# Kernel tuning notes

Hardware: AMD Instinct MI355X
Metric: run time of the kernel (lower is better)

The kernel has to match this reference:

```python
import jax, jax.numpy as jnp
import numpy as np

D_SPEC, D_PRE, D_CTX, D_H = 552, 256, 128, 1024


def _lstm_cell(x, h, c, Wih, Whh, bih, bhh):
    # PyTorch gate order: i, f, g, o
    g = x @ Wih.T + bih + h @ Whh.T + bhh
    i, f, gg, o = jnp.split(g, 4, axis=-1)
    c_new = jax.nn.sigmoid(f) * c + jax.nn.sigmoid(i) * jnp.tanh(gg)
    h_new = jax.nn.sigmoid(o) * jnp.tanh(c_new)
    return h_new, c_new


def _conv1d(x, w, b):
    # x: [B, C_in, L], w: [C_out, C_in, K], 'same' padding for K=5
    y = jax.lax.conv_general_dilated(x, w, window_strides=(1,), padding=[(2, 2)],
                                     dimension_numbers=('NCH', 'OIH', 'NCH'))
    return y + b[None, :, None]


def setup_inputs() -> dict:
    key = jax.random.key(0)
    ks = jax.random.split(key, 26)
    s = 0.05
    shapes = {
        'S_pad': (600, 64, D_SPEC),
        'pre_W1': (D_PRE, D_SPEC), 'pre_b1': (D_PRE,),
        'pre_W2': (D_PRE, D_PRE), 'pre_b2': (D_PRE,),
        'Wih0': (4 * D_H, D_PRE + D_CTX), 'Whh0': (4 * D_H, D_H),
        'bih0': (4 * D_H,), 'bhh0': (4 * D_H,),
        'Wih1': (4 * D_H, D_H), 'Whh1': (4 * D_H, D_H),
        'bih1': (4 * D_H,), 'bhh1': (4 * D_H,),
        'lin_W': (D_SPEC, D_H + D_CTX), 'lin_b': (D_SPEC,),
        'cw1': (512, D_SPEC, 5), 'cb1': (512,),
        'cw2': (512, 512, 5), 'cb2': (512,),
        'cw3': (512, 512, 5), 'cb3': (512,),
        'cw4': (512, 512, 5), 'cb4': (512,),
        'cw5': (D_SPEC, 512, 5), 'cb5': (D_SPEC,),
    }
    out = {}
    for i, (name, shp) in enumerate(shapes.items()):
        scale = 1.0 if name == 'S_pad' else s
        out[name] = scale * jax.random.normal(ks[i], shp, dtype=jnp.float32)
    return out


def reference(S_pad, pre_W1, pre_b1, pre_W2, pre_b2,
              Wih0, Whh0, bih0, bhh0, Wih1, Whh1, bih1, bhh1,
              lin_W, lin_b, cw1, cb1, cw2, cb2, cw3, cb3, cw4, cb4, cw5, cb5):
    L, B, _ = S_pad.shape
    # teacher forcing: input frame at t is S_pad[t-1] (zeros at t=0) -> precompute pre_net batched
    in_frames = jnp.concatenate([jnp.zeros((1, B, D_SPEC), S_pad.dtype), S_pad[:-1]], axis=0)
    pre = jax.nn.relu(in_frames @ pre_W1.T + pre_b1)
    pre = jax.nn.relu(pre @ pre_W2.T + pre_b2)  # dropout = identity (eval)
    ctx = jnp.zeros((L, B, D_CTX), S_pad.dtype)  # dummy_context
    lstm_in = jnp.concatenate([pre, ctx], axis=-1)  # [L, B, 384]

    h0 = jnp.zeros((B, D_H), S_pad.dtype)
    init = (h0, h0, h0, h0)  # (h0, c0, h1, c1)

    def step(carry, x):
        h0, c0, h1, c1 = carry
        h0, c0 = _lstm_cell(x, h0, c0, Wih0, Whh0, bih0, bhh0)
        h1, c1 = _lstm_cell(h0, h1, c1, Wih1, Whh1, bih1, bhh1)
        return (h0, c0, h1, c1), h1

    _, outs = jax.lax.scan(step, init, lstm_in)  # [L, B, 1024]
    S_pred = jnp.concatenate([outs, ctx], axis=-1) @ lin_W.T + lin_b  # [L, B, 552]

    x = jnp.transpose(S_pred, (1, 2, 0))  # [B, 552, L]
    x = jnp.tanh(_conv1d(x, cw1, cb1))
    x = jnp.tanh(_conv1d(x, cw2, cb2))
    x = jnp.tanh(_conv1d(x, cw3, cb3))
    x = jnp.tanh(_conv1d(x, cw4, cb4))
    x = _conv1d(x, cw5, cb5)
    S_residual = jnp.transpose(x, (2, 0, 1))  # [L, B, 552]
    return S_pred + S_residual
```

## Files before the change

### kernel.cpp

```cpp
#include <hip/hip_runtime.h>
#include <cstdint>
#include <cstddef>

typedef __bf16 bf16;
typedef __attribute__((ext_vector_type(8))) __bf16 bf16x8;
typedef __attribute__((ext_vector_type(4))) float f32x4;
typedef __attribute__((ext_vector_type(4))) unsigned u32x4;

#define DEV static __device__ __forceinline__

DEV float sigm_(float x) { return 1.f / (1.f + __expf(-x)); }
DEV float tanhf_(float x) {
  float e = __expf(-2.f * fabsf(x));
  float t = (1.f - e) / (1.f + e);
  return x < 0.f ? -t : t;
}

DEV void gload_lds16(const bf16* g, bf16* l) {
  __builtin_amdgcn_global_load_lds((const __attribute__((address_space(1))) void*)g,
                                   (__attribute__((address_space(3))) void*)l, 16, 0, 0);
}

__global__ void k_frames(const float* __restrict__ S, bf16* __restrict__ dst) {
  int idx = blockIdx.x * 256 + threadIdx.x;
  if (idx >= 38400 * 576) return;
  int r = idx / 576, c = idx - r * 576;
  int t = r >> 6, b = r & 63;
  float v = (t == 0 || c >= 552) ? 0.f : S[((size_t)(t - 1) * 64 + b) * 552 + c];
  dst[idx] = (bf16)v;
}

__global__ void k_pad2d(const float* __restrict__ src, bf16* __restrict__ dst,
                        int N, int Cdst, int Csrc, int Rsrc, int sstride) {
  int idx = blockIdx.x * 256 + threadIdx.x;
  if (idx >= N) return;
  int r = idx / Cdst, c = idx - r * Cdst;
  float v = (r < Rsrc && c < Csrc) ? src[(size_t)r * sstride + c] : 0.f;
  dst[idx] = (bf16)v;
}

__global__ void k_w0c(const float* __restrict__ Whh0, const float* __restrict__ Wih0,
                      bf16* __restrict__ dst) {
  int idx = blockIdx.x * 256 + threadIdx.x;
  if (idx >= 4096 * 1280) return;
  int r = idx / 1280, k = idx - r * 1280;
  float v = (k < 1024) ? Whh0[(size_t)r * 1024 + k] : Wih0[(size_t)r * 384 + (k - 1024)];
  dst[idx] = (bf16)v;
}

__global__ void k_w1c(const float* __restrict__ Wih1, const float* __restrict__ Whh1,
                      bf16* __restrict__ dst) {
  int idx = blockIdx.x * 256 + threadIdx.x;
  if (idx >= 4096 * 2048) return;
  int r = idx / 2048, k = idx - r * 2048;
  float v = (k < 1024) ? Wih1[(size_t)r * 1024 + k] : Whh1[(size_t)r * 1024 + (k - 1024)];
  dst[idx] = (bf16)v;
}

__global__ void k_convw(const float* __restrict__ src, bf16* __restrict__ dst,
                        int N, int Cpad, int Cisrc, int Cosrc) {
  int idx = blockIdx.x * 256 + threadIdx.x;
  if (idx >= N) return;
  int per = 5 * Cpad;
  int co = idx / per, rem = idx - co * per;
  int tap = rem / Cpad, ci = rem - tap * Cpad;
  float v = (co < Cosrc && ci < Cisrc) ? src[((size_t)co * Cisrc + ci) * 5 + tap] : 0.f;
  dst[idx] = (bf16)v;
}

__global__ void k_zpad(bf16* __restrict__ X0, bf16* __restrict__ X1, bf16* __restrict__ X2) {
  int idx = blockIdx.x * 256 + threadIdx.x;
  if (idx >= 64 * 4 * 1600) return;
  int per = 4 * 1600;
  int b = idx / per, rem = idx - b * per;
  int rr = rem / 1600, c = rem - rr * 1600;
  int row = (rr < 2) ? rr : 600 + rr;
  if (c < 576) X0[((size_t)b * 604 + row) * 576 + c] = (bf16)0.f;
  else if (c < 1088) X1[((size_t)b * 604 + row) * 512 + (c - 576)] = (bf16)0.f;
  else X2[((size_t)b * 604 + row) * 512 + (c - 1088)] = (bf16)0.f;
}

__global__ void k_sent(unsigned* __restrict__ C0u) {
  int idx = blockIdx.x * 256 + threadIdx.x;
  if (idx >= 600 * 64 * 512) return;
  int d = idx & 511;
  int rb = idx >> 9;
  int b = rb & 63, t1 = (rb >> 6) + 1;
  C0u[(size_t)t1 * 40960 + (size_t)b * 640 + d] = 0xFFFFFFFFu;
}

enum { M_RELU = 0, M_LINEAR = 1, M_CONVT = 2, M_CONVF = 3 };

template <int MODE>
__global__ __launch_bounds__(256) void gemm_k(
    const bf16* __restrict__ A, const bf16* __restrict__ B, int Ktot, int Kstride,
    int Brows, const float* __restrict__ bias,
    bf16* __restrict__ outB, int outStride, int colP, int colOff,
    float* __restrict__ outF, bf16* __restrict__ outX) {
  const int tid = threadIdx.x;
  const int lane = tid & 63, wv = tid >> 6;
  const int n0 = blockIdx.x * 128, m0 = blockIdx.y * 128;
  const int bz = blockIdx.z;
  __shared__ bf16 As[128 * 64];
  __shared__ bf16 Bs[128 * 64];
  f32x4 acc[4][4] = {};
  const int wr = wv >> 1, wc = wv & 1;
  int tap = 0, ci0 = 0;

  for (int kb = 0; kb < Ktot; kb += 64) {
#pragma unroll
    for (int j = 0; j < 4; ++j) {
      int rt = wv * 32 + j * 8 + (lane >> 3);
      const bf16* gp;
      if (MODE == M_CONVT || MODE == M_CONVF) {
        int l = m0 + rt;
        if (l > 599) l = 599;
        gp = A + ((size_t)(bz * 604 + l + tap)) * Kstride + ci0 + (lane & 7) * 8;
      } else {
        gp = A + (size_t)(m0 + rt) * Kstride + kb + (lane & 7) * 8;
      }
      gload_lds16(gp, &As[(wv * 32 + j * 8) * 64]);
    }
#pragma unroll
    for (int j = 0; j < 4; ++j) {
      int rn = n0 + wv * 32 + j * 8 + (lane >> 3);
      if (rn >= Brows) rn = Brows - 1;
      const bf16* gp = B + (size_t)rn * Ktot + kb + (lane & 7) * 8;
      gload_lds16(gp, &Bs[(wv * 32 + j * 8) * 64]);
    }
    __syncthreads();
#pragma unroll
    for (int ks = 0; ks < 2; ++ks) {
      const int ko = ks * 32 + (lane >> 4) * 8;
      bf16x8 af[4], bfr[4];
#pragma unroll
      for (int i = 0; i < 4; ++i) {
        af[i] = *(const bf16x8*)&As[(wr * 64 + i * 16 + (lane & 15)) * 64 + ko];
        bfr[i] = *(const bf16x8*)&Bs[(wc * 64 + i * 16 + (lane & 15)) * 64 + ko];
      }
#pragma unroll
      for (int mi = 0; mi < 4; ++mi)
#pragma unroll
        for (int ni = 0; ni < 4; ++ni)
          acc[mi][ni] = __builtin_amdgcn_mfma_f32_16x16x32_bf16(af[mi], bfr[ni], acc[mi][ni], 0, 0, 0);
    }
    __syncthreads();
    ci0 += 64;
    if (ci0 == Kstride) { ci0 = 0; ++tap; }
  }

  const int r0 = (lane >> 4) * 4, cc = lane & 15;
#pragma unroll
  for (int mi = 0; mi < 4; ++mi) {
#pragma unroll
    for (int ni = 0; ni < 4; ++ni) {
#pragma unroll
      for (int r = 0; r < 4; ++r) {
        float v = acc[mi][ni][r];
        int gr = m0 + wr * 64 + mi * 16 + r0 + r;
        int gc = n0 + wc * 64 + ni * 16 + cc;
        if (MODE == M_RELU) {
          v += bias[gc];
          v = fmaxf(v, 0.f);
          outB[(size_t)(gr >> 6) * outStride + (size_t)(gr & 63) * colP + colOff + gc] = (bf16)v;
        } else if (MODE == M_LINEAR) {
          if (gc < 552) {
            v += bias[gc];
            int t = gr >> 6, b = gr & 63;
            outF[(size_t)gr * 552 + gc] = v;
            outX[((size_t)b * 604 + t + 2) * 576 + gc] = (bf16)v;
          }
        } else if (MODE == M_CONVT) {
          if (gr < 600) {
            v = tanhf_(v + bias[gc]);
            outB[((size_t)bz * 604 + gr + 2) * 512 + gc] = (bf16)v;
          }
        } else {
          if (gr < 600 && gc < 552) {
            v += bias[gc];
            float* p = outF + ((size_t)gr * 64 + bz) * 552 + gc;
            *p += v;
          }
        }
      }
    }
  }
}

template <int LAYER>
DEV void scan_impl(bf16* __restrict__ C0, bf16* __restrict__ H1,
                   const bf16* __restrict__ W, const float* __restrict__ bi,
                   const float* __restrict__ bh, float* gb, int u0, int b0) {
  constexpr int KT = LAYER ? 2048 : 1280;
  constexpr int NKS = KT / 256;
  const int tid = threadIdx.x, lane = tid & 63, w = tid >> 6;
  const int kb = w * (KT / 8);

  bf16x8 wreg[4][NKS];
#pragma unroll
  for (int gi = 0; gi < 4; ++gi)
#pragma unroll
    for (int ks = 0; ks < NKS; ++ks)
      wreg[gi][ks] = *(const bf16x8*)(W + (size_t)(gi * 1024 + u0 + (lane & 15)) * KT +
                                      kb + ks * 32 + (lane >> 4) * 8);

  const int uc = tid & 15, bl = tid >> 4;
  float bs[4];
#pragma unroll
  for (int g = 0; g < 4; ++g) bs[g] = bi[g * 1024 + u0 + uc] + bh[g * 1024 + u0 + uc];
  float cst = 0.f;
  const int rotc = (bl + 4 * uc) & 31;

  const int r0 = lane & 15, q8 = (lane >> 4) * 8;
  const int un = lane & 15, qb = (lane >> 4) * 4;

  for (int t = 0; t < 600; ++t) {
    const bf16* A0;
    int RS;
    if (!LAYER) {
      RS = 1280;
      A0 = C0 + (size_t)t * 81920 + (size_t)(b0 + r0) * 1280 + kb + q8;
    } else if (w < 4) {
      RS = 1280;
      A0 = C0 + (size_t)(t + 1) * 81920 + (size_t)(b0 + r0) * 1280 + kb + q8;
    } else {
      RS = 1024;
      A0 = H1 + (size_t)(t + 1) * 65536 + (size_t)(b0 + r0) * 1024 + (kb - 1024) + q8;
    }
    const bf16* A1 = A0 + 16 * RS;

    u32x4 va[NKS], vb[NKS];
    if (!LAYER) {
#pragma unroll
      for (int ks = 0; ks < NKS; ++ks)
        if (kb + ks * 32 >= 1024) {
          va[ks] = *(const u32x4*)(A0 + ks * 32);
          vb[ks] = *(const u32x4*)(A1 + ks * 32);
        }
    }
    for (;;) {
#pragma unroll
      for (int ks = 0; ks < NKS; ++ks) {
        if (LAYER || kb + ks * 32 < 1024) {
          asm volatile("global_load_dwordx4 %0, %1, off sc0 sc1"
                       : "=v"(va[ks]) : "v"(A0 + ks * 32) : "memory");
          asm volatile("global_load_dwordx4 %0, %1, off sc0 sc1"
                       : "=v"(vb[ks]) : "v"(A1 + ks * 32) : "memory");
        }
      }
      asm volatile("s_waitcnt vmcnt(0)" ::: "memory");
      __builtin_amdgcn_sched_barrier(0);
      unsigned bad = 0;
#pragma unroll
      for (int ks = 0; ks < NKS; ++ks) {
        if (LAYER || kb + ks * 32 < 1024) {
          bad |= (va[ks].x == 0xFFFFFFFFu) | (va[ks].y == 0xFFFFFFFFu) |
                 (va[ks].z == 0xFFFFFFFFu) | (va[ks].w == 0xFFFFFFFFu) |
                 (vb[ks].x == 0xFFFFFFFFu) | (vb[ks].y == 0xFFFFFFFFu) |
                 (vb[ks].z == 0xFFFFFFFFu) | (vb[ks].w == 0xFFFFFFFFu);
        }
      }
      if (!__ballot(bad)) break;
      __builtin_amdgcn_s_sleep(2);
    }

    f32x4 acc[4][2] = {};
#pragma unroll
    for (int ks = 0; ks < NKS; ++ks) {
      bf16x8 a0 = *(const bf16x8*)&va[ks];
      bf16x8 a1 = *(const bf16x8*)&vb[ks];
#pragma unroll
      for (int gi = 0; gi < 4; ++gi) {
        acc[gi][0] = __builtin_amdgcn_mfma_f32_16x16x32_bf16(a0, wreg[gi][ks], acc[gi][0], 0, 0, 0);
        acc[gi][1] = __builtin_amdgcn_mfma_f32_16x16x32_bf16(a1, wreg[gi][ks], acc[gi][1], 0, 0, 0);
      }
    }

#pragma unroll
    for (int gi = 0; gi < 4; ++gi)
#pragma unroll
      for (int b2 = 0; b2 < 2; ++b2)
        *(f32x4*)&gb[((w * 4 + gi) * 16 + un) * 32 + ((b2 * 16 + qb + 4 * un) & 31)] = acc[gi][b2];

    asm volatile("s_waitcnt lgkmcnt(0)" ::: "memory");
    __builtin_amdgcn_s_barrier();
    __builtin_amdgcn_sched_barrier(0);

    float s4[4];
#pragma unroll
    for (int g = 0; g < 4; ++g) {
      float a = 0.f;
#pragma unroll
      for (int ww = 0; ww < 8; ++ww) a += gb[((ww * 4 + g) * 16 + uc) * 32 + rotc];
      s4[g] = a + bs[g];
    }
    float c = sigm_(s4[1]) * cst + sigm_(s4[0]) * tanhf_(s4[2]);
    cst = c;
    float h = sigm_(s4[3]) * tanhf_(c);

    float h1 = __shfl_down(h, 1), h2 = __shfl_down(h, 2), h3 = __shfl_down(h, 3);
    if ((uc & 3) == 0) {
      union { bf16 q[4]; unsigned long long u; } pk;
      pk.q[0] = (bf16)h; pk.q[1] = (bf16)h1; pk.q[2] = (bf16)h2; pk.q[3] = (bf16)h3;
      unsigned long long* dst = LAYER
          ? (unsigned long long*)(H1 + (size_t)(t + 2) * 65536 + (size_t)(b0 + bl) * 1024 + u0 + uc)
          : (unsigned long long*)(C0 + (size_t)(t + 1) * 81920 + (size_t)(b0 + bl) * 1280 + u0 + uc);
      __hip_atomic_store(dst, pk.u, __ATOMIC_RELAXED, __HIP_MEMORY_SCOPE_AGENT);
    }

    asm volatile("s_waitcnt lgkmcnt(0)" ::: "memory");
    __builtin_amdgcn_s_barrier();
    __builtin_amdgcn_sched_barrier(0);
  }
}

__global__ __launch_bounds__(512, 1) void lstm_k(
    bf16* __restrict__ C0, bf16* __restrict__ H1,
    const bf16* __restrict__ W0, const bf16* __restrict__ W1,
    const float* __restrict__ bi0, const float* __restrict__ bh0,
    const float* __restrict__ bi1, const float* __restrict__ bh1) {
  __shared__ float gb[512 * 32];
  const int bid = blockIdx.x;
  const int layer = bid >> 7, sub = bid & 127;
  const int mh = sub >> 6, ub = sub & 63;
  const int u0 = ub * 16, b0 = mh * 32;
  if (layer == 0)
    scan_impl<0>(C0, H1, W0, bi0, bh0, gb, u0, b0);
  else
    scan_impl<1>(C0, H1, W1, bi1, bh1, gb, u0, b0);
}

static inline unsigned gdiv(size_t n) { return (unsigned)((n + 255) / 256); }

extern "C" void kernel_launch(void* const* d_in, const int* in_sizes, int n_in,
                              void* d_out, int out_size, void* d_ws, size_t ws_size,
                              hipStream_t stream) {
  const float* S = (const float*)d_in[0];
  const float* preW1 = (const float*)d_in[1];
  const float* preb1 = (const float*)d_in[2];
  const float* preW2 = (const float*)d_in[3];
  const float* preb2 = (const float*)d_in[4];
  const float* Wih0 = (const float*)d_in[5];
  const float* Whh0 = (const float*)d_in[6];
  const float* bih0 = (const float*)d_in[7];
  const float* bhh0 = (const float*)d_in[8];
  const float* Wih1 = (const float*)d_in[9];
  const float* Whh1 = (const float*)d_in[10];
  const float* bih1 = (const float*)d_in[11];
  const float* bhh1 = (const float*)d_in[12];
  const float* linW = (const float*)d_in[13];
  const float* linb = (const float*)d_in[14];
  const float* cw1 = (const float*)d_in[15];
  const float* cb1 = (const float*)d_in[16];
  const float* cw2 = (const float*)d_in[17];
  const float* cb2 = (const float*)d_in[18];
  const float* cw3 = (const float*)d_in[19];
  const float* cb3 = (const float*)d_in[20];
  const float* cw4 = (const float*)d_in[21];
  const float* cb4 = (const float*)d_in[22];
  const float* cw5 = (const float*)d_in[23];
  const float* cb5 = (const float*)d_in[24];
  float* out = (float*)d_out;

  char* ws = (char*)d_ws;
  size_t off = 0;
  auto alloc = [&](size_t bytes) -> char* {
    char* p = ws + off;
    off += (bytes + 255) & ~(size_t)255;
    return p;
  };
  bf16* H1 = (bf16*)alloc(602ull * 64 * 1024 * 2);
  bf16* frames = (bf16*)alloc(38400ull * 576 * 2);
  bf16* pre1 = (bf16*)alloc(38400ull * 256 * 2);
  bf16* W0c = (bf16*)alloc(4096ull * 1280 * 2);
  bf16* W1c = (bf16*)alloc(4096ull * 2048 * 2);
  bf16* pW1b = (bf16*)alloc(256ull * 576 * 2);
  bf16* pW2b = (bf16*)alloc(256ull * 256 * 2);
  bf16* linWb = (bf16*)alloc(576ull * 1024 * 2);
  bf16* c1r = (bf16*)alloc(512ull * 5 * 576 * 2);
  bf16* c2r = (bf16*)alloc(512ull * 5 * 512 * 2);
  bf16* c3r = (bf16*)alloc(512ull * 5 * 512 * 2);
  bf16* c4r = (bf16*)alloc(512ull * 5 * 512 * 2);
  bf16* c5r = (bf16*)alloc(576ull * 5 * 512 * 2);
  bf16* X0 = (bf16*)alloc(64ull * 604 * 576 * 2);
  bf16* X1 = (bf16*)alloc(64ull * 604 * 512 * 2);
  bf16* X2 = (bf16*)alloc(64ull * 604 * 512 * 2);
  bf16* C0 = X0;

  hipMemsetAsync(H1, 0, 2ull * 64 * 1024 * 2, stream);
  hipMemsetAsync((char*)H1 + 2ull * 64 * 1024 * 2, 0xFF, 600ull * 64 * 1024 * 2, stream);
  hipMemsetAsync(C0, 0, 64ull * 1280 * 2, stream);
  k_sent<<<gdiv(600ull * 64 * 512), 256, 0, stream>>>((unsigned*)C0);

  k_frames<<<gdiv(38400ull * 576), 256, 0, stream>>>(S, frames);
  k_pad2d<<<gdiv(256 * 576), 256, 0, stream>>>(preW1, pW1b, 256 * 576, 576, 552, 256, 552);
  k_pad2d<<<gdiv(256 * 256), 256, 0, stream>>>(preW2, pW2b, 256 * 256, 256, 256, 256, 256);
  k_pad2d<<<gdiv(576 * 1024), 256, 0, stream>>>(linW, linWb, 576 * 1024, 1024, 1024, 552, 1152);
  k_w0c<<<gdiv(4096ull * 1280), 256, 0, stream>>>(Whh0, Wih0, W0c);
  k_w1c<<<gdiv(4096ull * 2048), 256, 0, stream>>>(Wih1, Whh1, W1c);
  k_convw<<<gdiv(512ull * 5 * 576), 256, 0, stream>>>(cw1, c1r, 512 * 5 * 576, 576, 552, 512);
  k_convw<<<gdiv(512ull * 5 * 512), 256, 0, stream>>>(cw2, c2r, 512 * 5 * 512, 512, 512, 512);
  k_convw<<<gdiv(512ull * 5 * 512), 256, 0, stream>>>(cw3, c3r, 512 * 5 * 512, 512, 512, 512);
  k_convw<<<gdiv(512ull * 5 * 512), 256, 0, stream>>>(cw4, c4r, 512 * 5 * 512, 512, 512, 512);
  k_convw<<<gdiv(576ull * 5 * 512), 256, 0, stream>>>(cw5, c5r, 576 * 5 * 512, 512, 512, 552);

  gemm_k<M_RELU><<<dim3(2, 300, 1), 256, 0, stream>>>(frames, pW1b, 576, 576, 256, preb1,
                                                      pre1, 16384, 256, 0, nullptr, nullptr);
  gemm_k<M_RELU><<<dim3(2, 300, 1), 256, 0, stream>>>(pre1, pW2b, 256, 256, 256, preb2,
                                                      C0, 81920, 1280, 1024, nullptr, nullptr);
  lstm_k<<<dim3(256), 512, 0, stream>>>(C0, H1, W0c, W1c, bih0, bhh0, bih1, bhh1);
  k_zpad<<<gdiv(64 * 4 * 1600), 256, 0, stream>>>(X0, X1, X2);
  gemm_k<M_LINEAR><<<dim3(5, 300, 1), 256, 0, stream>>>(H1 + 131072, linWb, 1024, 1024, 576, linb,
                                                        nullptr, 0, 0, 0, out, X0);
  gemm_k<M_CONVT><<<dim3(4, 5, 64), 256, 0, stream>>>(X0, c1r, 2880, 576, 512, cb1,
                                                      X1, 0, 0, 0, nullptr, nullptr);
  gemm_k<M_CONVT><<<dim3(4, 5, 64), 256, 0, stream>>>(X1, c2r, 2560, 512, 512, cb2,
                                                      X2, 0, 0, 0, nullptr, nullptr);
  gemm_k<M_CONVT><<<dim3(4, 5, 64), 256, 0, stream>>>(X2, c3r, 2560, 512, 512, cb3,
                                                      X1, 0, 0, 0, nullptr, nullptr);
  gemm_k<M_CONVT><<<dim3(4, 5, 64), 256, 0, stream>>>(X1, c4r, 2560, 512, 512, cb4,
                                                      X2, 0, 0, 0, nullptr, nullptr);
  gemm_k<M_CONVF><<<dim3(5, 5, 64), 256, 0, stream>>>(X2, c5r, 2560, 512, 576, cb5,
                                                      nullptr, 0, 0, 0, out, nullptr);
  (void)in_sizes; (void)n_in; (void)out_size; (void)ws_size;
}
```

Before: 5.133 ms.

## Replace sentinel-polling with per-block progress flags in persistent LSTM scan

The persistent LSTM kernel previously waited on its inputs by repeatedly reloading the full h-vector slices with cache-bypassing loads until no 0xFFFFFFFF sentinel remained, which required prefilling C0 and H1 with sentinels. Now each block publishes a per-timestep counter flag after its h stores have drained, and consumer waves spin only on a small set of flags before doing ordinary loads of the activations. This removes the sentinel prefill kernel and the large memset, and cuts polling traffic. The risk is memory ordering: flag stores are relaxed and follow only a vmcnt wait, and the later loads are ordinary rather than cache-bypassing, so stale data may be read.

Result: faster. 4.978 ms (-3.0%).

```diff
diff --git a/kernel.cpp b/kernel.cpp
--- a/kernel.cpp
+++ b/kernel.cpp
@@ -78,15 +78,6 @@
   if (c < 576) X0[((size_t)b * 604 + row) * 576 + c] = (bf16)0.f;
   else if (c < 1088) X1[((size_t)b * 604 + row) * 512 + (c - 576)] = (bf16)0.f;
   else X2[((size_t)b * 604 + row) * 512 + (c - 1088)] = (bf16)0.f;
-}
-
-__global__ void k_sent(unsigned* __restrict__ C0u) {
-  int idx = blockIdx.x * 256 + threadIdx.x;
-  if (idx >= 600 * 64 * 512) return;
-  int d = idx & 511;
-  int rb = idx >> 9;
-  int b = rb & 63, t1 = (rb >> 6) + 1;
-  C0u[(size_t)t1 * 40960 + (size_t)b * 640 + d] = 0xFFFFFFFFu;
 }
 
 enum { M_RELU = 0, M_LINEAR = 1, M_CONVT = 2, M_CONVF = 3 };
@@ -190,7 +181,8 @@
 template <int LAYER>
 DEV void scan_impl(bf16* __restrict__ C0, bf16* __restrict__ H1,
                    const bf16* __restrict__ W, const float* __restrict__ bi,
-                   const float* __restrict__ bh, float* gb, int u0, int b0) {
+                   const float* __restrict__ bh, unsigned* __restrict__ flags,
+                   float* gb, int u0, int b0, int mh, int ub) {
   constexpr int KT = LAYER ? 2048 : 1280;
   constexpr int NKS = KT / 256;
   const int tid = threadIdx.x, lane = tid & 63, w = tid >> 6;
@@ -211,10 +203,36 @@
   float cst = 0.f;
   const int rotc = (bl + 4 * uc) & 31;
 
+  unsigned* flO = flags + (LAYER * 2 + mh) * 64 * 32;
+  unsigned* flP = flags + mh * 64 * 32;
+
+  const unsigned* fl;
+  int fb, nf, thrAdd;
+  if (!LAYER) {
+    fl = flO; fb = w * 10; nf = (w < 6) ? 10 : (w == 6 ? 4 : 0); thrAdd = 0;
+  } else if (w < 4) {
+    fl = flP; fb = w * 16; nf = 16; thrAdd = 1;
+  } else {
+    fl = flO; fb = (w - 4) * 16; nf = 16; thrAdd = 0;
+  }
+
   const int r0 = lane & 15, q8 = (lane >> 4) * 8;
   const int un = lane & 15, qb = (lane >> 4) * 4;
 
   for (int t = 0; t < 600; ++t) {
+    if (nf && (LAYER || t > 0)) {
+      const unsigned thr = (unsigned)(t + thrAdd);
+      for (;;) {
+        unsigned f = (lane < nf)
+            ? __hip_atomic_load(&fl[(fb + lane) << 5], __ATOMIC_RELAXED, __HIP_MEMORY_SCOPE_AGENT)
+            : 0xFFFFFFFFu;
+        if (!__ballot(f < thr)) break;
+        __builtin_amdgcn_s_sleep(1);
+      }
+      __builtin_amdgcn_sched_barrier(0);
+      asm volatile("" ::: "memory");
+    }
+
     const bf16* A0;
     int RS;
     if (!LAYER) {
@@ -229,46 +247,11 @@
     }
     const bf16* A1 = A0 + 16 * RS;
 
-    u32x4 va[NKS], vb[NKS];
-    if (!LAYER) {
-#pragma unroll
-      for (int ks = 0; ks < NKS; ++ks)
-        if (kb + ks * 32 >= 1024) {
-          va[ks] = *(const u32x4*)(A0 + ks * 32);
-          vb[ks] = *(const u32x4*)(A1 + ks * 32);
-        }
-    }
-    for (;;) {
-#pragma unroll
-      for (int ks = 0; ks < NKS; ++ks) {
-        if (LAYER || kb + ks * 32 < 1024) {
-          asm volatile("global_load_dwordx4 %0, %1, off sc0 sc1"
-                       : "=v"(va[ks]) : "v"(A0 + ks * 32) : "memory");
-          asm volatile("global_load_dwordx4 %0, %1, off sc0 sc1"
-                       : "=v"(vb[ks]) : "v"(A1 + ks * 32) : "memory");
-        }
-      }
-      asm volatile("s_waitcnt vmcnt(0)" ::: "memory");
-      __builtin_amdgcn_sched_barrier(0);
-      unsigned bad = 0;
-#pragma unroll
-      for (int ks = 0; ks < NKS; ++ks) {
-        if (LAYER || kb + ks * 32 < 1024) {
-          bad |= (va[ks].x == 0xFFFFFFFFu) | (va[ks].y == 0xFFFFFFFFu) |
-                 (va[ks].z == 0xFFFFFFFFu) | (va[ks].w == 0xFFFFFFFFu) |
-                 (vb[ks].x == 0xFFFFFFFFu) | (vb[ks].y == 0xFFFFFFFFu) |
-                 (vb[ks].z == 0xFFFFFFFFu) | (vb[ks].w == 0xFFFFFFFFu);
-        }
-      }
-      if (!__ballot(bad)) break;
-      __builtin_amdgcn_s_sleep(2);
-    }
-
     f32x4 acc[4][2] = {};
 #pragma unroll
     for (int ks = 0; ks < NKS; ++ks) {
-      bf16x8 a0 = *(const bf16x8*)&va[ks];
-      bf16x8 a1 = *(const bf16x8*)&vb[ks];
+      bf16x8 a0 = *(const bf16x8*)(A0 + ks * 32);
+      bf16x8 a1 = *(const bf16x8*)(A1 + ks * 32);
 #pragma unroll
       for (int gi = 0; gi < 4; ++gi) {
         acc[gi][0] = __builtin_amdgcn_mfma_f32_16x16x32_bf16(a0, wreg[gi][ks], acc[gi][0], 0, 0, 0);
@@ -307,10 +290,11 @@
           : (unsigned long long*)(C0 + (size_t)(t + 1) * 81920 + (size_t)(b0 + bl) * 1280 + u0 + uc);
       __hip_atomic_store(dst, pk.u, __ATOMIC_RELAXED, __HIP_MEMORY_SCOPE_AGENT);
     }
-
-    asm volatile("s_waitcnt lgkmcnt(0)" ::: "memory");
+    asm volatile("s_waitcnt vmcnt(0)" ::: "memory");
     __builtin_amdgcn_s_barrier();
     __builtin_amdgcn_sched_barrier(0);
+    if (tid == 0)
+      __hip_atomic_store(&flO[ub << 5], (unsigned)(t + 1), __ATOMIC_RELAXED, __HIP_MEMORY_SCOPE_AGENT);
   }
 }
 
@@ -318,16 +302,17 @@
     bf16* __restrict__ C0, bf16* __restrict__ H1,
     const bf16* __restrict__ W0, const bf16* __restrict__ W1,
     const float* __restrict__ bi0, const float* __restrict__ bh0,
-    const float* __restrict__ bi1, const float* __restrict__ bh1) {
+    const float* __restrict__ bi1, const float* __restrict__ bh1,
+    unsigned* __restrict__ flags) {
   __shared__ float gb[512 * 32];
   const int bid = blockIdx.x;
   const int layer = bid >> 7, sub = bid & 127;
   const int mh = sub >> 6, ub = sub & 63;
   const int u0 = ub * 16, b0 = mh * 32;
   if (layer == 0)
-    scan_impl<0>(C0, H1, W0, bi0, bh0, gb, u0, b0);
+    scan_impl<0>(C0, H1, W0, bi0, bh0, flags, gb, u0, b0, mh, ub);
   else
-    scan_impl<1>(C0, H1, W1, bi1, bh1, gb, u0, b0);
+    scan_impl<1>(C0, H1, W1, bi1, bh1, flags, gb, u0, b0, mh, ub);
 }
 
 static inline unsigned gdiv(size_t n) { return (unsigned)((n + 255) / 256); }
@@ -369,6 +354,7 @@
     off += (bytes + 255) & ~(size_t)255;
     return p;
   };
+  unsigned* flags = (unsigned*)alloc(32768);
   bf16* H1 = (bf16*)alloc(602ull * 64 * 1024 * 2);
   bf16* frames = (bf16*)alloc(38400ull * 576 * 2);
   bf16* pre1 = (bf16*)alloc(38400ull * 256 * 2);
@@ -387,10 +373,8 @@
   bf16* X2 = (bf16*)alloc(64ull * 604 * 512 * 2);
   bf16* C0 = X0;
 
-  hipMemsetAsync(H1, 0, 2ull * 64 * 1024 * 2, stream);
-  hipMemsetAsync((char*)H1 + 2ull * 64 * 1024 * 2, 0xFF, 600ull * 64 * 1024 * 2, stream);
+  hipMemsetAsync(ws, 0, 32768 + 2ull * 64 * 1024 * 2, stream);
   hipMemsetAsync(C0, 0, 64ull * 1280 * 2, stream);
-  k_sent<<<gdiv(600ull * 64 * 512), 256, 0, stream>>>((unsigned*)C0);
 
   k_frames<<<gdiv(38400ull * 576), 256, 0, stream>>>(S, frames);
   k_pad2d<<<gdiv(256 * 576), 256, 0, stream>>>(preW1, pW1b, 256 * 576, 576, 552, 256, 552);
@@ -408,7 +392,7 @@
                                                       pre1, 16384, 256, 0, nullptr, nullptr);
   gemm_k<M_RELU><<<dim3(2, 300, 1), 256, 0, stream>>>(pre1, pW2b, 256, 256, 256, preb2,
                                                       C0, 81920, 1280, 1024, nullptr, nullptr);
-  lstm_k<<<dim3(256), 512, 0, stream>>>(C0, H1, W0c, W1c, bih0, bhh0, bih1, bhh1);
+  lstm_k<<<dim3(256), 512, 0, stream>>>(C0, H1, W0c, W1c, bih0, bhh0, bih1, bhh1, flags);
   k_zpad<<<gdiv(64 * 4 * 1600), 256, 0, stream>>>(X0, X1, X2);
   gemm_k<M_LINEAR><<<dim3(5, 300, 1), 256, 0, stream>>>(H1 + 131072, linWb, 1024, 1024, 576, linb,
                                                         nullptr, 0, 0, 0, out, X0);
```

## Add per-block progress flags to LSTM scan and interleave block-to-layer mapping

Applied to the files above, without the earlier changes.

Each LSTM block now publishes a per-timestep progress flag, set by the last wave to arrive through an LDS counter. Consumers poll the small set of producer flags before issuing plain loads, and fall back to the old sentinel-polling loop only if stale data is seen. The block-to-(layer, batch half, unit) mapping is also interleaved so the groups spread across CUs and XCDs differently. This replaces repeated uncached polling of whole activation tiles with cheap flag polling, at the cost of extra atomics and a memory-ordering risk between the relaxed data stores and the relaxed flag store.

Result: slower. 5.291 ms (+3.1%).

```diff
diff --git a/kernel.cpp b/kernel.cpp
--- a/kernel.cpp
+++ b/kernel.cpp
@@ -190,7 +190,8 @@
 template <int LAYER>
 DEV void scan_impl(bf16* __restrict__ C0, bf16* __restrict__ H1,
                    const bf16* __restrict__ W, const float* __restrict__ bi,
-                   const float* __restrict__ bh, float* gb, int u0, int b0) {
+                   const float* __restrict__ bh, unsigned* __restrict__ flags,
+                   float* gb, unsigned* cnt, int u0, int b0, int mh, int ub) {
   constexpr int KT = LAYER ? 2048 : 1280;
   constexpr int NKS = KT / 256;
   const int tid = threadIdx.x, lane = tid & 63, w = tid >> 6;
@@ -211,10 +212,39 @@
   float cst = 0.f;
   const int rotc = (bl + 4 * uc) & 31;
 
+  unsigned* flO = flags + (LAYER * 2 + mh) * 64 * 32;
+  unsigned* flP = flags + mh * 64 * 32;
+
+  const unsigned* fl;
+  int fb, nf, thrAdd;
+  if (!LAYER) {
+    fl = flO; fb = w * 10; nf = (w < 6) ? 10 : (w == 6 ? 4 : 0); thrAdd = 0;
+  } else if (w < 4) {
+    fl = flP; fb = w * 16; nf = 16; thrAdd = 1;
+  } else {
+    fl = flO; fb = (w - 4) * 16; nf = 16; thrAdd = 0;
+  }
+
+  if (tid == 0) *cnt = 0u;
+  __syncthreads();
+
   const int r0 = lane & 15, q8 = (lane >> 4) * 8;
   const int un = lane & 15, qb = (lane >> 4) * 4;
 
   for (int t = 0; t < 600; ++t) {
+    if (nf && (LAYER || t > 0)) {
+      const unsigned thr = (unsigned)(t + thrAdd);
+      for (;;) {
+        unsigned f = (lane < nf)
+            ? __hip_atomic_load(&fl[(fb + lane) << 5], __ATOMIC_RELAXED, __HIP_MEMORY_SCOPE_AGENT)
+            : 0xFFFFFFFFu;
+        if (!__ballot(f < thr)) break;
+        __builtin_amdgcn_s_sleep(1);
+      }
+      __builtin_amdgcn_sched_barrier(0);
+      asm volatile("" ::: "memory");
+    }
+
     const bf16* A0;
     int RS;
     if (!LAYER) {
@@ -230,38 +260,47 @@
     const bf16* A1 = A0 + 16 * RS;
 
     u32x4 va[NKS], vb[NKS];
-    if (!LAYER) {
-#pragma unroll
-      for (int ks = 0; ks < NKS; ++ks)
-        if (kb + ks * 32 >= 1024) {
-          va[ks] = *(const u32x4*)(A0 + ks * 32);
-          vb[ks] = *(const u32x4*)(A1 + ks * 32);
+#pragma unroll
+    for (int ks = 0; ks < NKS; ++ks) {
+      va[ks] = *(const u32x4*)(A0 + ks * 32);
+      vb[ks] = *(const u32x4*)(A1 + ks * 32);
+    }
+    unsigned bad = 0;
+#pragma unroll
+    for (int ks = 0; ks < NKS; ++ks) {
+      if (LAYER || kb + ks * 32 < 1024) {
+        bad |= (va[ks].x == 0xFFFFFFFFu) | (va[ks].y == 0xFFFFFFFFu) |
+               (va[ks].z == 0xFFFFFFFFu) | (va[ks].w == 0xFFFFFFFFu) |
+               (vb[ks].x == 0xFFFFFFFFu) | (vb[ks].y == 0xFFFFFFFFu) |
+               (vb[ks].z == 0xFFFFFFFFu) | (vb[ks].w == 0xFFFFFFFFu);
+      }
+    }
+    if (__ballot(bad)) {
+      for (;;) {
+#pragma unroll
+        for (int ks = 0; ks < NKS; ++ks) {
+          if (LAYER || kb + ks * 32 < 1024) {
+            asm volatile("global_load_dwordx4 %0, %1, off sc0 sc1"
+                         : "=v"(va[ks]) : "v"(A0 + ks * 32) : "memory");
+            asm volatile("global_load_dwordx4 %0, %1, off sc0 sc1"
+                         : "=v"(vb[ks]) : "v"(A1 + ks * 32) : "memory");
+          }
         }
-    }
-    for (;;) {
-#pragma unroll
-      for (int ks = 0; ks < NKS; ++ks) {
-        if (LAYER || kb + ks * 32 < 1024) {
-          asm volatile("global_load_dwordx4 %0, %1, off sc0 sc1"
-                       : "=v"(va[ks]) : "v"(A0 + ks * 32) : "memory");
-          asm volatile("global_load_dwordx4 %0, %1, off sc0 sc1"
-                       : "=v"(vb[ks]) : "v"(A1 + ks * 32) : "memory");
+        asm volatile("s_waitcnt vmcnt(0)" ::: "memory");
+        __builtin_amdgcn_sched_barrier(0);
+        unsigned bad2 = 0;
+#pragma unroll
+        for (int ks = 0; ks < NKS; ++ks) {
+          if (LAYER || kb + ks * 32 < 1024) {
+            bad2 |= (va[ks].x == 0xFFFFFFFFu) | (va[ks].y == 0xFFFFFFFFu) |
+                    (va[ks].z == 0xFFFFFFFFu) | (va[ks].w == 0xFFFFFFFFu) |
+                    (vb[ks].x == 0xFFFFFFFFu) | (vb[ks].y == 0xFFFFFFFFu) |
+                    (vb[ks].z == 0xFFFFFFFFu) | (vb[ks].w == 0xFFFFFFFFu);
+          }
         }
-      }
-      asm volatile("s_waitcnt vmcnt(0)" ::: "memory");
-      __builtin_amdgcn_sched_barrier(0);
-      unsigned bad = 0;
-#pragma unroll
-      for (int ks = 0; ks < NKS; ++ks) {
-        if (LAYER || kb + ks * 32 < 1024) {
-          bad |= (va[ks].x == 0xFFFFFFFFu) | (va[ks].y == 0xFFFFFFFFu) |
-                 (va[ks].z == 0xFFFFFFFFu) | (va[ks].w == 0xFFFFFFFFu) |
-                 (vb[ks].x == 0xFFFFFFFFu) | (vb[ks].y == 0xFFFFFFFFu) |
-                 (vb[ks].z == 0xFFFFFFFFu) | (vb[ks].w == 0xFFFFFFFFu);
-        }
-      }
-      if (!__ballot(bad)) break;
-      __builtin_amdgcn_s_sleep(2);
+        if (!__ballot(bad2)) break;
+        __builtin_amdgcn_s_sleep(1);
+      }
     }
 
     f32x4 acc[4][2] = {};
@@ -308,7 +347,12 @@
       __hip_atomic_store(dst, pk.u, __ATOMIC_RELAXED, __HIP_MEMORY_SCOPE_AGENT);
     }
 
-    asm volatile("s_waitcnt lgkmcnt(0)" ::: "memory");
+    if (lane == 0) {
+      unsigned o = atomicAdd(cnt, 1u);
+      if (o == (unsigned)(8 * t + 7))
+        __hip_atomic_store(&flO[ub << 5], (unsigned)(t + 1), __ATOMIC_RELAXED,
+                           __HIP_MEMORY_SCOPE_AGENT);
+    }
     __builtin_amdgcn_s_barrier();
     __builtin_amdgcn_sched_barrier(0);
   }
@@ -318,16 +362,19 @@
     bf16* __restrict__ C0, bf16* __restrict__ H1,
     const bf16* __restrict__ W0, const bf16* __restrict__ W1,
     const float* __restrict__ bi0, const float* __restrict__ bh0,
-    const float* __restrict__ bi1, const float* __restrict__ bh1) {
+    const float* __restrict__ bi1, const float* __restrict__ bh1,
+    unsigned* __restrict__ flags) {
   __shared__ float gb[512 * 32];
+  __shared__ unsigned cnt;
   const int bid = blockIdx.x;
-  const int layer = bid >> 7, sub = bid & 127;
-  const int mh = sub >> 6, ub = sub & 63;
+  const int g = (bid & 7) >> 1;
+  const int ub = ((bid >> 3) << 1) | (bid & 1);
+  const int layer = g >> 1, mh = g & 1;
   const int u0 = ub * 16, b0 = mh * 32;
   if (layer == 0)
-    scan_impl<0>(C0, H1, W0, bi0, bh0, gb, u0, b0);
+    scan_impl<0>(C0, H1, W0, bi0, bh0, flags, gb, &cnt, u0, b0, mh, ub);
   else
-    scan_impl<1>(C0, H1, W1, bi1, bh1, gb, u0, b0);
+    scan_impl<1>(C0, H1, W1, bi1, bh1, flags, gb, &cnt, u0, b0, mh, ub);
 }
 
 static inline unsigned gdiv(size_t n) { return (unsigned)((n + 255) / 256); }
@@ -369,6 +416,7 @@
     off += (bytes + 255) & ~(size_t)255;
     return p;
   };
+  unsigned* flags = (unsigned*)alloc(32768);
   bf16* H1 = (bf16*)alloc(602ull * 64 * 1024 * 2);
   bf16* frames = (bf16*)alloc(38400ull * 576 * 2);
   bf16* pre1 = (bf16*)alloc(38400ull * 256 * 2);
@@ -387,7 +435,7 @@
   bf16* X2 = (bf16*)alloc(64ull * 604 * 512 * 2);
   bf16* C0 = X0;
 
-  hipMemsetAsync(H1, 0, 2ull * 64 * 1024 * 2, stream);
+  hipMemsetAsync(ws, 0, 32768 + 2ull * 64 * 1024 * 2, stream);
   hipMemsetAsync((char*)H1 + 2ull * 64 * 1024 * 2, 0xFF, 600ull * 64 * 1024 * 2, stream);
   hipMemsetAsync(C0, 0, 64ull * 1280 * 2, stream);
   k_sent<<<gdiv(600ull * 64 * 512), 256, 0, stream>>>((unsigned*)C0);
@@ -408,7 +456,7 @@
                                                       pre1, 16384, 256, 0, nullptr, nullptr);
   gemm_k<M_RELU><<<dim3(2, 300, 1), 256, 0, stream>>>(pre1, pW2b, 256, 256, 256, preb2,
                                                       C0, 81920, 1280, 1024, nullptr, nullptr);
-  lstm_k<<<dim3(256), 512, 0, stream>>>(C0, H1, W0c, W1c, bih0, bhh0, bih1, bhh1);
+  lstm_k<<<dim3(256), 512, 0, stream>>>(C0, H1, W0c, W1c, bih0, bhh0, bih1, bhh1, flags);
   k_zpad<<<gdiv(64 * 4 * 1600), 256, 0, stream>>>(X0, X1, X2);
   gemm_k<M_LINEAR><<<dim3(5, 300, 1), 256, 0, stream>>>(H1 + 131072, linWb, 1024, 1024, 576, linb,
                                                         nullptr, 0, 0, 0, out, X0);
```
